# Optimization experiments

Hardware: AMD Instinct MI355X
Metric: run time of the kernel (lower is better)

The kernel has to match this reference:

```python
import jax, jax.numpy as jnp
import numpy as np

B, S, T = 4, 4096, 512
D_MODEL, D_TEXT = 1024, 768
H, KVH, HD = 16, 2, 64  # heads, kv heads, head_dim; rep = H // KVH
REP = H // KVH
EPS = 1e-5


def setup_inputs() -> dict:
    key = jax.random.key(0)
    k = jax.random.split(key, 6)
    std = 0.02
    return {
        "x": jax.random.normal(k[0], (B, S, D_MODEL), jnp.float32),
        "text_input": jax.random.normal(k[1], (B, T, D_TEXT), jnp.float32),
        "ln_w": jnp.ones((D_TEXT,), jnp.float32),
        "ln_b": jnp.zeros((D_TEXT,), jnp.float32),
        # weights stored as [in, out] (transposed torch Linear layout)
        "Wq": jax.random.normal(k[2], (D_MODEL, D_MODEL), jnp.float32) * std,
        "Wkv": jax.random.normal(k[3], (D_TEXT, 2 * KVH * HD), jnp.float32) * std,
        "Wout": jax.random.normal(k[4], (D_MODEL, D_MODEL), jnp.float32) * std,
        "bout": jnp.zeros((D_MODEL,), jnp.float32),
    }


def reference(x, text_input, ln_w, ln_b, Wq, Wkv, Wout, bout):
    # LayerNorm over d_text
    mu = jnp.mean(text_input, axis=-1, keepdims=True)
    var = jnp.var(text_input, axis=-1, keepdims=True)
    tn = (text_input - mu) * jax.lax.rsqrt(var + EPS) * ln_w + ln_b

    # Projections
    Q = (x @ Wq).reshape(B, S, KVH, REP, HD)          # heads are kv-major: h = g*REP + r
    KV = tn @ Wkv                                      # [B, T, 2*KVH*HD]
    K, V = jnp.split(KV, 2, axis=-1)
    K = K.reshape(B, T, KVH, HD)
    V = V.reshape(B, T, KVH, HD)

    # Grouped-query attention without materializing repeated K/V
    scale = 1.0 / np.sqrt(HD)
    scores = jnp.einsum('bsgrd,btgd->bgrst', Q, K) * scale  # [B,KVH,REP,S,T]
    attn = jax.nn.softmax(scores, axis=-1)
    O = jnp.einsum('bgrst,btgd->bsgrd', attn, V).reshape(B, S, D_MODEL)

    return O @ Wout + bout
```

## Files before the change

### kernel.cpp

```cpp
#include <hip/hip_runtime.h>
#include <hip/hip_bf16.h>


#define B_    4
#define S_    4096
#define T_    512
#define DM_   1024
#define DT_   768
#define H_    16
#define KVH_  2
#define HD_   64

#define GLOBAL_AS __attribute__((address_space(1)))
#define LDS_AS    __attribute__((address_space(3)))

typedef __bf16 bf16x8 __attribute__((ext_vector_type(8)));
typedef float  f32x4  __attribute__((ext_vector_type(4)));

__global__ __launch_bounds__(256) void cast_f32_bf16(const float* __restrict__ in,
                                                     __hip_bfloat16* __restrict__ out) {
    int i = blockIdx.x * 256 + threadIdx.x;
    float4 v = ((const float4*)in)[i];
    union { ushort4 u; __hip_bfloat16 h[4]; } p;
    p.h[0] = __float2bfloat16(v.x);
    p.h[1] = __float2bfloat16(v.y);
    p.h[2] = __float2bfloat16(v.z);
    p.h[3] = __float2bfloat16(v.w);
    ((ushort4*)out)[i] = p.u;
}

__global__ __launch_bounds__(256) void transpose_cast(const float* __restrict__ in,
                                                      __hip_bfloat16* __restrict__ out,
                                                      int R, int C) {
    __shared__ float tile[32][33];
    int tx = threadIdx.x, ty = threadIdx.y;
    int r0 = blockIdx.y * 32, c0 = blockIdx.x * 32;
#pragma unroll
    for (int k = 0; k < 4; k++)
        tile[ty + 8 * k][tx] = in[(size_t)(r0 + ty + 8 * k) * C + c0 + tx];
    __syncthreads();
#pragma unroll
    for (int k = 0; k < 4; k++)
        out[(size_t)(c0 + ty + 8 * k) * R + r0 + tx] = __float2bfloat16(tile[tx][ty + 8 * k]);
}

__global__ __launch_bounds__(256) void ln_norm(const float* __restrict__ text,
                                               const float* __restrict__ lnw,
                                               const float* __restrict__ lnb,
                                               __hip_bfloat16* __restrict__ tnb) {
    int tid = threadIdx.x;
    int w = tid >> 6, lane = tid & 63;
    int row0 = blockIdx.x * 8 + w * 2;
#pragma unroll
    for (int rr = 0; rr < 2; ++rr) {
        int row = row0 + rr;
        const float4* src = (const float4*)(text + (size_t)row * DT_);
        float4 v[3];
        float s = 0.f, s2 = 0.f;
#pragma unroll
        for (int j = 0; j < 3; ++j) {
            v[j] = src[lane + 64 * j];
            s  += v[j].x + v[j].y + v[j].z + v[j].w;
            s2 += v[j].x * v[j].x + v[j].y * v[j].y + v[j].z * v[j].z + v[j].w * v[j].w;
        }
#pragma unroll
        for (int ofs = 1; ofs < 64; ofs <<= 1) {
            s  += __shfl_xor(s, ofs);
            s2 += __shfl_xor(s2, ofs);
        }
        float mu  = s * (1.0f / DT_);
        float var = s2 * (1.0f / DT_) - mu * mu;
        float rs  = rsqrtf(var + 1e-5f);
#pragma unroll
        for (int j = 0; j < 3; ++j) {
            float4 wv = ((const float4*)lnw)[lane + 64 * j];
            float4 bv = ((const float4*)lnb)[lane + 64 * j];
            union { ushort4 u; __hip_bfloat16 h[4]; } p;
            p.h[0] = __float2bfloat16((v[j].x - mu) * rs * wv.x + bv.x);
            p.h[1] = __float2bfloat16((v[j].y - mu) * rs * wv.y + bv.y);
            p.h[2] = __float2bfloat16((v[j].z - mu) * rs * wv.z + bv.z);
            p.h[3] = __float2bfloat16((v[j].w - mu) * rs * wv.w + bv.w);
            ((ushort4*)(tnb + (size_t)row * DT_))[lane + 64 * j] = p.u;
        }
    }
}

__global__ __launch_bounds__(256) void kv_gemm(const __hip_bfloat16* __restrict__ Atn,
                                               const __hip_bfloat16* __restrict__ Wkvt,
                                               __hip_bfloat16* __restrict__ Kg,
                                               __hip_bfloat16* __restrict__ Vt) {
    __shared__ __bf16 As[2][64 * 32];
    __shared__ __bf16 Bs[2][64 * 32];
    const int tid = threadIdx.x;
    const int w = tid >> 6, lane = tid & 63, q = lane >> 4, cL = lane & 15;
    const size_t m0 = (size_t)blockIdx.y * 64, n0 = (size_t)blockIdx.x * 64;
    const int K = DT_;
    const int NT = K / 32;

    int srcoff, dstoff;
    {
        int id = tid;
        int sr = id >> 3, U = (id & 7) ^ (sr & 7);
        int row = 2 * sr + (U >> 2), ko = (U & 3) * 8;
        srcoff = row * K + ko;
        dstoff = id * 8;
    }
    const __bf16* Ab = (const __bf16*)Atn + m0 * K;
    const __bf16* Bb = (const __bf16*)Wkvt + n0 * K;

    auto frag_off = [&](int R) {
        return (R >> 1) * 64 + ((((R & 1) * 4 + q) ^ ((R >> 1) & 7)) * 8);
    };
    const int offA = frag_off(w * 16 + cL);
    int offB[4];
#pragma unroll
    for (int nf = 0; nf < 4; ++nf) offB[nf] = frag_off(nf * 16 + cL);

    f32x4 acc[4] = {};

    auto STAGE = [&](int buf, int t) {
        int k0 = t * 32;
        __builtin_amdgcn_global_load_lds((const GLOBAL_AS void*)(Ab + srcoff + k0),
                                         (LDS_AS void*)(&As[buf][dstoff]), 16, 0, 0);
        __builtin_amdgcn_global_load_lds((const GLOBAL_AS void*)(Bb + srcoff + k0),
                                         (LDS_AS void*)(&Bs[buf][dstoff]), 16, 0, 0);
    };

    STAGE(0, 0);
    __syncthreads();
    for (int t = 0; t < NT; ++t) {
        int cur = t & 1;
        if (t + 1 < NT) STAGE(cur ^ 1, t + 1);
        bf16x8 af = *(const bf16x8*)&As[cur][offA];
#pragma unroll
        for (int nf = 0; nf < 4; ++nf) {
            bf16x8 bf = *(const bf16x8*)&Bs[cur][offB[nf]];
            acc[nf] = __builtin_amdgcn_mfma_f32_16x16x32_bf16(af, bf, acc[nf], 0, 0, 0);
        }
        __syncthreads();
    }

#pragma unroll
    for (int nf = 0; nf < 4; ++nf) {
        int n = (int)n0 + nf * 16 + cL;
        int isV = n >> 7, g = (n >> 6) & 1, d = n & 63;
#pragma unroll
        for (int ii = 0; ii < 4; ++ii) {
            int m = (int)m0 + w * 16 + 4 * q + ii;
            int b = m >> 9, tt = m & 511;
            __hip_bfloat16 hv = __float2bfloat16(acc[nf][ii]);
            if (!isV) Kg[((size_t)(b * KVH_ + g) * T_ + tt) * HD_ + d] = hv;
            else      Vt[((size_t)(b * KVH_ + g) * HD_ + d) * T_ + tt] = hv;
        }
    }
}

template <int EPI>
__global__ __launch_bounds__(512, 2) void gemm256(const __hip_bfloat16* __restrict__ A,
                                                  const __hip_bfloat16* __restrict__ Bt,
                                                  void* __restrict__ Cout,
                                                  const float* __restrict__ bias,
                                                  float scale, int M, int N, int K) {
    __shared__ __bf16 lds[65536];
    const int tid = threadIdx.x;
    const int w = tid >> 6, lane = tid & 63, q = lane >> 4, cL = lane & 15;
    const int wm = w >> 2, wn = w & 3;
    const size_t m0 = (size_t)blockIdx.y * 256, n0 = (size_t)blockIdx.x * 256;
    const __bf16* Ab = (const __bf16*)A + m0 * K;
    const __bf16* Bb = (const __bf16*)Bt + n0 * K;
    const int NT = K >> 6;

    int srcoff[2], dstoff[2];
#pragma unroll
    for (int it = 0; it < 2; ++it) {
        int id = tid + it * 512;
        int r = id >> 3, u = (id & 7) ^ (r & 7);
        srcoff[it] = r * K + u * 8;
        dstoff[it] = id * 8;
    }

    const int swz0 = ((0 + q) ^ (cL & 7)) * 8;
    const int swz1 = ((4 + q) ^ (cL & 7)) * 8;
    const int baseA = (wm * 128 + cL) * 64;
    const int baseB = (wn * 64 + cL) * 64;

    f32x4 acc[8][4] = {};

    auto STAGE = [&](int isB, int j, int tt) {
        const __bf16* g = (isB ? Bb : Ab) + (size_t)j * 128 * K + (size_t)tt * 64;
        const int sb = (tt & 1) * 32768 + isB * 16384 + j * 8192;
#pragma unroll
        for (int it = 0; it < 2; ++it)
            __builtin_amdgcn_global_load_lds(
                (const GLOBAL_AS void*)(g + srcoff[it]),
                (LDS_AS void*)(&lds[sb + dstoff[it]]), 16, 0, 0);
    };

    STAGE(0, 0, 0); STAGE(0, 1, 0); STAGE(1, 0, 0); STAGE(1, 1, 0);
    if (NT > 1) { STAGE(0, 0, 1); STAGE(0, 1, 1); }
    asm volatile("s_waitcnt vmcnt(4)" ::: "memory");
    __builtin_amdgcn_s_barrier();
    __builtin_amdgcn_sched_barrier(0);

    for (int t = 0; t < NT; ++t) {
        const int sb = (t & 1) * 32768;
        const __bf16* As = lds + sb;
        const __bf16* Bs = lds + sb + 16384;
        bf16x8 af[4][2];
#pragma unroll
        for (int ph = 0; ph < 4; ++ph) {
            const int mh = ph >> 1, nh = ph & 1;
            if (nh == 0) {
#pragma unroll
                for (int m = 0; m < 4; ++m) {
                    int ro = baseA + mh * 4096 + m * 1024;
                    af[m][0] = *(const bf16x8*)&As[ro + swz0];
                    af[m][1] = *(const bf16x8*)&As[ro + swz1];
                }
            }
            bf16x8 bq[2][2];
#pragma unroll
            for (int n = 0; n < 2; ++n) {
                int ro = baseB + nh * 2048 + n * 1024;
                bq[n][0] = *(const bf16x8*)&Bs[ro + swz0];
                bq[n][1] = *(const bf16x8*)&Bs[ro + swz1];
            }
            if (ph == 0)      { if (t + 1 < NT) STAGE(1, 0, t + 1); }
            else if (ph == 1) { if (t + 1 < NT) STAGE(1, 1, t + 1); }
            else if (ph == 3 && t + 2 < NT) { STAGE(0, 0, t + 2); STAGE(0, 1, t + 2); }

            __builtin_amdgcn_s_barrier();
            __builtin_amdgcn_sched_barrier(0);
            __builtin_amdgcn_s_setprio(1);
#pragma unroll
            for (int m = 0; m < 4; ++m)
#pragma unroll
                for (int n = 0; n < 2; ++n) {
                    f32x4* a = &acc[mh * 4 + m][nh * 2 + n];
                    *a = __builtin_amdgcn_mfma_f32_16x16x32_bf16(af[m][0], bq[n][0], *a, 0, 0, 0);
                    *a = __builtin_amdgcn_mfma_f32_16x16x32_bf16(af[m][1], bq[n][1], *a, 0, 0, 0);
                }
            __builtin_amdgcn_s_setprio(0);
            if (ph == 3) {
                if (t + 2 < NT)      asm volatile("s_waitcnt vmcnt(4)" ::: "memory");
                else if (t + 1 < NT) asm volatile("s_waitcnt vmcnt(0)" ::: "memory");
            }
            __builtin_amdgcn_s_barrier();
            __builtin_amdgcn_sched_barrier(0);
        }
    }

#pragma unroll
    for (int jn = 0; jn < 4; ++jn) {
        size_t col = n0 + wn * 64 + jn * 16 + cL;
        float bb = 0.0f;
        if (EPI == 1) bb = bias[col];
#pragma unroll
        for (int im = 0; im < 8; ++im) {
            size_t r = m0 + wm * 128 + im * 16 + 4 * q;
#pragma unroll
            for (int ii = 0; ii < 4; ++ii) {
                float v = acc[im][jn][ii];
                if (EPI == 0)
                    ((__hip_bfloat16*)Cout)[(r + ii) * N + col] = __float2bfloat16(v * scale);
                else
                    ((float*)Cout)[(r + ii) * N + col] = v + bb;
            }
        }
    }
}

__global__ __launch_bounds__(256, 2) void attn_kernel(const __hip_bfloat16* __restrict__ Qs,
                                                      const __hip_bfloat16* __restrict__ Kg,
                                                      const __hip_bfloat16* __restrict__ Vt,
                                                      __hip_bfloat16* __restrict__ Oc) {
    __shared__ __bf16 Ks[2][64 * 64];
    __shared__ __bf16 Vs[2][64 * 64];
    __shared__ __bf16 Ps[4][2048];
    int tid = threadIdx.x;
    int w = tid >> 6, lane = tid & 63, q = lane >> 4, cL = lane & 15;
    int bh = blockIdx.y;
    int b = bh >> 4, h = bh & 15, g = h >> 3;
    int s0 = blockIdx.x * 256 + w * 64;

    const __bf16* Qb = (const __bf16*)Qs;
    const __bf16* Kb = (const __bf16*)Kg + (size_t)(b * KVH_ + g) * T_ * HD_;
    const __bf16* Vb = (const __bf16*)Vt + (size_t)(b * KVH_ + g) * HD_ * T_;
    __bf16* pw = &Ps[w][0];

    int ksoff[2], vsoff[2];
#pragma unroll
    for (int it = 0; it < 2; it++) {
        int U = tid + it * 256;
        int r = U >> 3, us = (U & 7) ^ (r & 7);
        ksoff[it] = r * HD_ + us * 8;
        vsoff[it] = r * T_  + us * 8;
    }

    auto STAGE = [&](int bufi, int tc) {
        int t0 = tc * 64;
#pragma unroll
        for (int it = 0; it < 2; it++) {
            int U = tid + it * 256;
            __builtin_amdgcn_global_load_lds(
                (const GLOBAL_AS void*)(Kb + (size_t)t0 * HD_ + ksoff[it]),
                (LDS_AS void*)(&Ks[bufi][U * 8]), 16, 0, 0);
            __builtin_amdgcn_global_load_lds(
                (const GLOBAL_AS void*)(Vb + t0 + vsoff[it]),
                (LDS_AS void*)(&Vs[bufi][U * 8]), 16, 0, 0);
        }
    };

    bf16x8 aq[4][2];
#pragma unroll
    for (int mi = 0; mi < 4; mi++) {
        size_t base = ((size_t)(b * S_) + s0 + mi * 16 + cL) * DM_ + h * HD_ + 8 * q;
        aq[mi][0] = *(const bf16x8*)(Qb + base);
        aq[mi][1] = *(const bf16x8*)(Qb + base + 32);
    }

    float lpart[4][4] = {};
    f32x4 oacc[4][4] = {};

    STAGE(0, 0);
    __syncthreads();
#pragma unroll 1
    for (int tc = 0; tc < 8; tc++) {
        int bufi = tc & 1;
        if (tc + 1 < 8) STAGE(bufi ^ 1, tc + 1);

#pragma unroll
        for (int ksc = 0; ksc < 2; ksc++) {
            f32x4 sc[4][2];
            __builtin_amdgcn_s_setprio(1);
#pragma unroll
            for (int half = 0; half < 2; half++) {
                int nt = 2 * ksc + half;
                int R = 16 * nt + cL;
                bf16x8 k0 = *(const bf16x8*)&Ks[bufi][R * 64 + ((q ^ (R & 7)) * 8)];
                bf16x8 k1 = *(const bf16x8*)&Ks[bufi][R * 64 + (((4 + q) ^ (R & 7)) * 8)];
#pragma unroll
                for (int mi = 0; mi < 4; mi++) {
                    f32x4 a = {0.f, 0.f, 0.f, 0.f};
                    a = __builtin_amdgcn_mfma_f32_16x16x32_bf16(aq[mi][0], k0, a, 0, 0, 0);
                    a = __builtin_amdgcn_mfma_f32_16x16x32_bf16(aq[mi][1], k1, a, 0, 0, 0);
                    sc[mi][half] = a;
                }
            }
            __builtin_amdgcn_s_setprio(0);

#pragma unroll
            for (int mi = 0; mi < 4; mi++)
#pragma unroll
                for (int i = 0; i < 4; i++) {
                    float e0 = __expf(sc[mi][0][i]); sc[mi][0][i] = e0;
                    float e1 = __expf(sc[mi][1][i]); sc[mi][1][i] = e1;
                    lpart[mi][i] += e0 + e1;
                }

#pragma unroll
            for (int mi = 0; mi < 4; mi++)
#pragma unroll
                for (int half = 0; half < 2; half++) {
                    int tin = half * 16 + cL;
                    int off = mi * 512 + (((tin >> 3) * 16 + 4 * q) * 8) + (tin & 7);
#pragma unroll
                    for (int i = 0; i < 4; i++)
                        pw[off + i * 8] = (__bf16)sc[mi][half][i];
                }
            bf16x8 pa[4];
#pragma unroll
            for (int mi = 0; mi < 4; mi++)
                pa[mi] = *(const bf16x8*)&pw[mi * 512 + lane * 8];

            __builtin_amdgcn_s_setprio(1);
#pragma unroll
            for (int nd = 0; nd < 4; nd++) {
                int D = 16 * nd + cL;
                bf16x8 bv = *(const bf16x8*)&Vs[bufi][D * 64 + (((4 * ksc + q) ^ (D & 7)) * 8)];
#pragma unroll
                for (int mi = 0; mi < 4; mi++)
                    oacc[mi][nd] = __builtin_amdgcn_mfma_f32_16x16x32_bf16(pa[mi], bv, oacc[mi][nd], 0, 0, 0);
            }
            __builtin_amdgcn_s_setprio(0);
        }
        __syncthreads();
    }

#pragma unroll
    for (int mi = 0; mi < 4; mi++) {
        float rinv[4];
#pragma unroll
        for (int i = 0; i < 4; i++) {
            float l = lpart[mi][i];
            l += __shfl_xor(l, 1); l += __shfl_xor(l, 2);
            l += __shfl_xor(l, 4); l += __shfl_xor(l, 8);
            rinv[i] = 1.0f / l;
        }
#pragma unroll
        for (int nd = 0; nd < 4; nd++)
#pragma unroll
            for (int i = 0; i < 4; i++) {
                float v = oacc[mi][nd][i] * rinv[i];
                size_t s = (size_t)(b * S_) + s0 + mi * 16 + 4 * q + i;
                Oc[s * DM_ + h * HD_ + nd * 16 + cL] = __float2bfloat16(v);
            }
    }
}

extern "C" void kernel_launch(void* const* d_in, const int* in_sizes, int n_in,
                              void* d_out, int out_size, void* d_ws, size_t ws_size,
                              hipStream_t stream) {
    const float* x    = (const float*)d_in[0];
    const float* text = (const float*)d_in[1];
    const float* lnw  = (const float*)d_in[2];
    const float* lnb  = (const float*)d_in[3];
    const float* Wq   = (const float*)d_in[4];
    const float* Wkv  = (const float*)d_in[5];
    const float* Wout = (const float*)d_in[6];
    const float* bout = (const float*)d_in[7];

    char* ws = (char*)d_ws;
    __hip_bfloat16* xbf = (__hip_bfloat16*)(ws);
    __hip_bfloat16* Qs  = (__hip_bfloat16*)(ws + 33554432);
    __hip_bfloat16* Wqt = (__hip_bfloat16*)(ws + 67108864);
    __hip_bfloat16* Wot = (__hip_bfloat16*)(ws + 69206016);
    __hip_bfloat16* Kg  = (__hip_bfloat16*)(ws + 71303168);
    __hip_bfloat16* Vtp = (__hip_bfloat16*)(ws + 71827456);
    __hip_bfloat16* tnb  = (__hip_bfloat16*)(ws + 33554432);
    __hip_bfloat16* Wkvt = (__hip_bfloat16*)(ws + 33554432 + 3145728);

    cast_f32_bf16<<<dim3((B_ * S_ * DM_) / 4 / 256), dim3(256), 0, stream>>>(x, xbf);
    transpose_cast<<<dim3(32, 32), dim3(32, 8), 0, stream>>>(Wq, Wqt, DM_, DM_);
    transpose_cast<<<dim3(32, 32), dim3(32, 8), 0, stream>>>(Wout, Wot, DM_, DM_);
    transpose_cast<<<dim3(8, 24), dim3(32, 8), 0, stream>>>(Wkv, Wkvt, DT_, 2 * KVH_ * HD_);

    ln_norm<<<dim3(B_ * T_ / 8), dim3(256), 0, stream>>>(text, lnw, lnb, tnb);

    kv_gemm<<<dim3(2 * KVH_ * HD_ / 64, B_ * T_ / 64), dim3(256), 0, stream>>>(
        tnb, Wkvt, Kg, Vtp);

    gemm256<0><<<dim3(DM_ / 256, (B_ * S_) / 256), dim3(512), 0, stream>>>(
        xbf, Wqt, (void*)Qs, nullptr, 0.125f, B_ * S_, DM_, DM_);

    attn_kernel<<<dim3(S_ / 256, B_ * H_), dim3(256), 0, stream>>>(Qs, Kg, Vtp, xbf);

    gemm256<1><<<dim3(DM_ / 256, (B_ * S_) / 256), dim3(512), 0, stream>>>(
        xbf, Wot, d_out, bout, 1.0f, B_ * S_, DM_, DM_);
}
```

Before: 303.8 us.

## Read K/V fragments directly from global memory in attention, drop LDS staging

```diff
diff --git a/kernel.cpp b/kernel.cpp
--- a/kernel.cpp
+++ b/kernel.cpp
@@ -270,12 +270,10 @@
     }
 }
 
-__global__ __launch_bounds__(256, 2) void attn_kernel(const __hip_bfloat16* __restrict__ Qs,
+__global__ __launch_bounds__(256, 4) void attn_kernel(const __hip_bfloat16* __restrict__ Qs,
                                                       const __hip_bfloat16* __restrict__ Kg,
                                                       const __hip_bfloat16* __restrict__ Vt,
                                                       __hip_bfloat16* __restrict__ Oc) {
-    __shared__ __bf16 Ks[2][64 * 64];
-    __shared__ __bf16 Vs[2][64 * 64];
     __shared__ __bf16 Ps[4][2048];
     int tid = threadIdx.x;
     int w = tid >> 6, lane = tid & 63, q = lane >> 4, cL = lane & 15;
@@ -288,29 +286,6 @@
     const __bf16* Vb = (const __bf16*)Vt + (size_t)(b * KVH_ + g) * HD_ * T_;
     __bf16* pw = &Ps[w][0];
 
-    int ksoff[2], vsoff[2];
-#pragma unroll
-    for (int it = 0; it < 2; it++) {
-        int U = tid + it * 256;
-        int r = U >> 3, us = (U & 7) ^ (r & 7);
-        ksoff[it] = r * HD_ + us * 8;
-        vsoff[it] = r * T_  + us * 8;
-    }
-
-    auto STAGE = [&](int bufi, int tc) {
-        int t0 = tc * 64;
-#pragma unroll
-        for (int it = 0; it < 2; it++) {
-            int U = tid + it * 256;
-            __builtin_amdgcn_global_load_lds(
-                (const GLOBAL_AS void*)(Kb + (size_t)t0 * HD_ + ksoff[it]),
-                (LDS_AS void*)(&Ks[bufi][U * 8]), 16, 0, 0);
-            __builtin_amdgcn_global_load_lds(
-                (const GLOBAL_AS void*)(Vb + t0 + vsoff[it]),
-                (LDS_AS void*)(&Vs[bufi][U * 8]), 16, 0, 0);
-        }
-    };
-
     bf16x8 aq[4][2];
 #pragma unroll
     for (int mi = 0; mi < 4; mi++) {
@@ -322,12 +297,10 @@
     float lpart[4][4] = {};
     f32x4 oacc[4][4] = {};
 
-    STAGE(0, 0);
-    __syncthreads();
 #pragma unroll 1
     for (int tc = 0; tc < 8; tc++) {
-        int bufi = tc & 1;
-        if (tc + 1 < 8) STAGE(bufi ^ 1, tc + 1);
+        const __bf16* Kc = Kb + (size_t)(tc * 64) * HD_;
+        const __bf16* Vc = Vb + tc * 64;
 
 #pragma unroll
         for (int ksc = 0; ksc < 2; ksc++) {
@@ -337,8 +310,8 @@
             for (int half = 0; half < 2; half++) {
                 int nt = 2 * ksc + half;
                 int R = 16 * nt + cL;
-                bf16x8 k0 = *(const bf16x8*)&Ks[bufi][R * 64 + ((q ^ (R & 7)) * 8)];
-                bf16x8 k1 = *(const bf16x8*)&Ks[bufi][R * 64 + (((4 + q) ^ (R & 7)) * 8)];
+                bf16x8 k0 = *(const bf16x8*)(Kc + (size_t)R * HD_ + 8 * q);
+                bf16x8 k1 = *(const bf16x8*)(Kc + (size_t)R * HD_ + 32 + 8 * q);
 #pragma unroll
                 for (int mi = 0; mi < 4; mi++) {
                     f32x4 a = {0.f, 0.f, 0.f, 0.f};
@@ -377,14 +350,13 @@
 #pragma unroll
             for (int nd = 0; nd < 4; nd++) {
                 int D = 16 * nd + cL;
-                bf16x8 bv = *(const bf16x8*)&Vs[bufi][D * 64 + (((4 * ksc + q) ^ (D & 7)) * 8)];
+                bf16x8 bv = *(const bf16x8*)(Vc + (size_t)D * T_ + 32 * ksc + 8 * q);
 #pragma unroll
                 for (int mi = 0; mi < 4; mi++)
                     oacc[mi][nd] = __builtin_amdgcn_mfma_f32_16x16x32_bf16(pa[mi], bv, oacc[mi][nd], 0, 0, 0);
             }
             __builtin_amdgcn_s_setprio(0);
         }
-        __syncthreads();
     }
 
 #pragma unroll
```

Result: slower. 555.7 us (+82.9%).
